# Performance work log

Measured on AMD Instinct MI355X. Metric: run time of the kernel, lower is better.

## Reference

```python
import jax, jax.numpy as jnp
import numpy as np

H = 16   # num_heads
G = 4    # groups (code structurally requires 4)
DIM = 1024
HD = DIM // H // G  # 16


def setup_inputs() -> dict:
    key = jax.random.key(0)
    k1, k2, k3 = jax.random.split(key, 3)
    x = jax.random.normal(k1, (8, 4096, DIM), dtype=jnp.float32)
    w_qkvw = jax.random.normal(k2, (DIM, 4 * DIM), dtype=jnp.float32) * 0.02
    w_out = jax.random.normal(k3, (DIM, DIM), dtype=jnp.float32) * 0.02
    return {"x": x, "w_qkvw": w_qkvw, "w_out": w_out}


def reference(x, w_qkvw, w_out):
    B, S, dim = x.shape
    qkvw = x @ w_qkvw  # [B, S, 4*dim]
    # chunk into G groups along last dim -> G tensors of [B, S, dim] (G==4)
    chunks = jnp.split(qkvw, G, axis=-1)
    # each chunk split again into G sub-chunks of [B, S, dim/G]
    subs = [jnp.split(t, G, axis=-1) for t in chunks]
    # torch: q,k,v,w = [cat([qi,ki,vi,wi], dim=0) for qi,ki,vi,wi in zip(*subs)]
    q = jnp.concatenate([subs[i][0] for i in range(4)], axis=0)  # [4B, S, dim/G]
    k = jnp.concatenate([subs[i][1] for i in range(4)], axis=0)
    v = jnp.concatenate([subs[i][2] for i in range(4)], axis=0)
    w = jnp.concatenate([subs[i][3] for i in range(4)], axis=0)
    # faithful row-major reshape: [4B, S, dim/G] -> [4B, H, S, hd] -> transpose(1,2)
    def shp(t):
        return t.reshape(B * G, H, -1, HD).swapaxes(1, 2)  # [4B, S, H, hd]
    q, k, v = shp(q), shp(k), shp(v)
    w = w.reshape(B * G, H, -1, HD)  # [4B, H, S, hd]
    scale = HD ** -0.5
    scores = (q @ k.swapaxes(-2, -1)) * scale          # [4B, S, H, H]
    attn = jax.nn.softmax(scores, axis=-1)
    o = (attn @ v).swapaxes(1, 2).reshape(B, S, dim)   # [B, S, dim]
    return (o * w.reshape(B, S, dim)) @ w_out
```

## Files before the change

kernel.cpp:

```cpp
#include <hip/hip_runtime.h>
#include <hip/hip_bf16.h>
#include <stdint.h>


typedef __bf16 bf16;
typedef __bf16 bf16x8 __attribute__((ext_vector_type(8)));
typedef float f32x4 __attribute__((ext_vector_type(4)));

__device__ __forceinline__ void gload16(const bf16* g, bf16* l) {
  __builtin_amdgcn_global_load_lds(
      (const __attribute__((address_space(1))) void*)g,
      (__attribute__((address_space(3))) void*)l, 16, 0, 0);
}

#define BAR() asm volatile("s_barrier" ::: "memory")
#define SB() __builtin_amdgcn_sched_barrier(0)
#define LGKM0 asm volatile("s_waitcnt lgkmcnt(0)" ::: "memory")
#define VM4 asm volatile("s_waitcnt vmcnt(4)" ::: "memory")
#define VM0 asm volatile("s_waitcnt vmcnt(0)" ::: "memory")
#define PRIO1 __builtin_amdgcn_s_setprio(1)
#define PRIO0 __builtin_amdgcn_s_setprio(0)

#define READ_A8(dst, base, mq)                                                \
  {                                                                           \
    _Pragma("unroll") for (int i = 0; i < 4; ++i)                             \
        _Pragma("unroll") for (int kk = 0; kk < 2; ++kk)                      \
            dst[i][kk] = *(const bf16x8*)(lds + (base) + ahalf +              \
                                          ((mq)*64 + i * 16 + fr) * 128 +     \
                                          ((kk * 64 + fkb) ^ xo));            \
  }
#define READ_B4(base, nh)                                                     \
  {                                                                           \
    _Pragma("unroll") for (int j2 = 0; j2 < 2; ++j2)                          \
        _Pragma("unroll") for (int kk = 0; kk < 2; ++kk)                      \
            b[(nh)*2 + j2][kk] = *(const bf16x8*)(lds + (base) + bhalf +      \
                                                  (bro + (nh)*32 + j2 * 16 + fr) * 128 + \
                                                  ((kk * 64 + fkb) ^ xo));    \
  }
#define MFMA_Q(arr, mq, nh)                                                   \
  {                                                                           \
    _Pragma("unroll") for (int i = 0; i < 4; ++i)                             \
        _Pragma("unroll") for (int j2 = 0; j2 < 2; ++j2) {                    \
      acc[(mq)*4 + i][(nh)*2 + j2] = __builtin_amdgcn_mfma_f32_16x16x32_bf16( \
          arr[i][0], b[(nh)*2 + j2][0], acc[(mq)*4 + i][(nh)*2 + j2], 0, 0, 0); \
      acc[(mq)*4 + i][(nh)*2 + j2] = __builtin_amdgcn_mfma_f32_16x16x32_bf16( \
          arr[i][1], b[(nh)*2 + j2][1], acc[(mq)*4 + i][(nh)*2 + j2], 0, 0, 0); \
    }                                                                         \
  }
#define STAGE(gsrc, lbase)                                                    \
  {                                                                           \
    gload16((gsrc), (bf16*)(lds + (lbase) + wv * 1024));                      \
    gload16((gsrc) + 64 * 1024, (bf16*)(lds + (lbase) + 8192 + wv * 1024));   \
  }

template <typename OutT>
__global__ __launch_bounds__(512, 2)
void gemm256(const bf16* __restrict__ A, const bf16* __restrict__ BT,
             OutT* __restrict__ C, int N, int super) {
  constexpr int K = 1024;
  __shared__ __align__(16) char smem[131072];
  char* lds = smem;

  const int tid = threadIdx.x;
  const int lane = tid & 63;
  const int wv = tid >> 6;
  const int wr = wv >> 2;
  const int wc = wv & 3;

  const int gx = gridDim.x;
  const int nwg = gx * gridDim.y;
  const int bid = blockIdx.y * gx + blockIdx.x;
  const int xcd = bid & 7;
  const int l = bid >> 3;
  long trow, tcol;
  if (super) {
    const int s = l >> 5, i = l & 31;
    const int colS = gx >> 2;
    trow = xcd * 16 + (s / colS) * 8 + (i >> 2);
    tcol = (s % colS) * 4 + (i & 3);
  } else {
    const int swz = xcd * (nwg >> 3) + l;
    trow = swz / gx;
    tcol = swz % gx;
  }
  const long row0 = trow * 256;
  const long col0 = tcol * 256;

  const int srow = tid >> 3;
  const int scol = (((tid & 7) * 16) ^ ((srow & 7) << 4)) >> 1;
  const bf16* gA = A + (row0 + srow) * K + scol;
  const bf16* gB = BT + (col0 + srow) * K + scol;

  const int fr = lane & 15;
  const int fkb = (lane >> 4) * 16;
  const int xo = (fr & 7) << 4;
  const int bro = (wc & 1) * 64;
  const int ahalf = wr * 16384;
  const int bhalf = (wc >> 1) * 16384;

  bf16x8 a0[4][2], a1[4][2], b[4][2];
  f32x4 acc[8][4] = {};

  STAGE(gA, 0); STAGE(gA + 131072, 16384);
  STAGE(gB, 65536); STAGE(gB + 131072, 81920);
  STAGE(gA + 64, 32768); STAGE(gA + 131072 + 64, 49152);
  VM4;
  SB(); BAR(); SB();

  const bf16* gAm = gA;
  const bf16* gBm = gB;
  for (int j = 0; j < 8; ++j) {
    const bool nl = (j < 7);
    READ_A8(a0, 0, 0); READ_B4(65536, 0);
    STAGE(gBm + 64, 98304);
    SB(); BAR(); LGKM0; SB();
    PRIO1; MFMA_Q(a0, 0, 0); PRIO0; SB(); BAR();
    READ_A8(a1, 0, 1);
    STAGE(gBm + 131072 + 64, 114688);
    SB(); BAR(); LGKM0; SB();
    PRIO1; MFMA_Q(a1, 1, 0); PRIO0; SB(); BAR();
    READ_B4(65536, 1);
    if (nl) STAGE(gAm + 128, 0);
    SB(); BAR(); LGKM0; SB();
    PRIO1; MFMA_Q(a1, 1, 1); PRIO0; SB(); BAR();
    if (nl) {
      STAGE(gAm + 131072 + 128, 16384);
      VM4;
    } else {
      VM0;
    }
    SB(); BAR(); LGKM0; SB();
    PRIO1; MFMA_Q(a0, 0, 1); PRIO0; SB(); BAR();
    READ_A8(a0, 32768, 0); READ_B4(98304, 0);
    if (nl) STAGE(gBm + 128, 65536);
    SB(); BAR(); LGKM0; SB();
    PRIO1; MFMA_Q(a0, 0, 0); PRIO0; SB(); BAR();
    READ_A8(a1, 32768, 1);
    if (nl) STAGE(gBm + 131072 + 128, 81920);
    SB(); BAR(); LGKM0; SB();
    PRIO1; MFMA_Q(a1, 1, 0); PRIO0; SB(); BAR();
    READ_B4(98304, 1);
    if (nl) STAGE(gAm + 192, 32768);
    SB(); BAR(); LGKM0; SB();
    PRIO1; MFMA_Q(a1, 1, 1); PRIO0; SB(); BAR();
    if (nl) {
      STAGE(gAm + 131072 + 192, 49152);
      VM4;
    }
    SB(); BAR(); LGKM0; SB();
    PRIO1; MFMA_Q(a0, 0, 1); PRIO0; SB(); BAR();
    gAm += 128;
    gBm += 128;
  }

  const int crow = (lane >> 4) * 4;
  const int ccol = lane & 15;
  const long rb = row0 + wr * 128;
  const long cb = col0 + wc * 64;
#pragma unroll
  for (int m = 0; m < 8; ++m)
#pragma unroll
    for (int n = 0; n < 4; ++n)
#pragma unroll
      for (int i = 0; i < 4; ++i)
        C[(rb + m * 16 + crow + i) * (long)N + cb + n * 16 + ccol] =
            (OutT)acc[m][n][i];
}

__device__ __forceinline__ void load16f(const bf16* p, float* f) {
  const uint4* u = (const uint4*)p;
  uint4 a = u[0], b = u[1];
  uint32_t w[8] = {a.x, a.y, a.z, a.w, b.x, b.y, b.z, b.w};
#pragma unroll
  for (int j = 0; j < 8; ++j) {
    f[2 * j] = __uint_as_float(w[j] << 16);
    f[2 * j + 1] = __uint_as_float(w[j] & 0xffff0000u);
  }
}

__global__ __launch_bounds__(256)
void attn_fuse(const bf16* __restrict__ qkvw, bf16* __restrict__ ow,
               int b0, long bstride) {
  __shared__ bf16 data[16 * 1024];
  const int s_hi = blockIdx.x;
  const int g = blockIdx.y;
  const int bz = blockIdx.z;
  const int b = b0 + bz;
  const bf16* base = qkvw + (long)bz * bstride;
  const int tid = threadIdx.x;

#pragma unroll
  for (int i = 0; i < 8; ++i) {
    int c = tid + i * 256;
    int h = c >> 7;
    int col = (c & 127) * 8;
    *(uint4*)&data[h * 1024 + col] =
        *(const uint4*)(base + (long)(h * 256 + s_hi) * 4096 + g * 1024 + col);
  }
  __syncthreads();

  const int s_lo = tid >> 4;
  const int h1 = tid & 15;
  const int off = s_lo * 16;

  float q[16], p[16], o[16];
  load16f(&data[h1 * 1024 + off], q);

  float mx = -1e30f;
#pragma unroll
  for (int h2 = 0; h2 < 16; ++h2) {
    float kf[16];
    load16f(&data[h2 * 1024 + 256 + off], kf);
    float s = 0.f;
#pragma unroll
    for (int d = 0; d < 16; ++d) s += q[d] * kf[d];
    s *= 0.25f;
    p[h2] = s;
    mx = fmaxf(mx, s);
  }
  float sum = 0.f;
#pragma unroll
  for (int h2 = 0; h2 < 16; ++h2) {
    float e = __expf(p[h2] - mx);
    p[h2] = e;
    sum += e;
  }
  const float inv = 1.f / sum;
#pragma unroll
  for (int d = 0; d < 16; ++d) o[d] = 0.f;
#pragma unroll
  for (int h2 = 0; h2 < 16; ++h2) {
    float vf[16];
    load16f(&data[h2 * 1024 + 512 + off], vf);
    const float av = p[h2] * inv;
#pragma unroll
    for (int d = 0; d < 16; ++d) o[d] += av * vf[d];
  }
  float wf[16];
  load16f(&data[h1 * 1024 + 768 + off], wf);

  const int bp = g * 8 + b;
  const long R = (long)(bp >> 2) * 4096 + (bp & 3) * 1024 + h1 * 64 + (s_hi >> 2);
  const int cbo = (s_hi & 3) * 256 + off;
  union { uint4 u[2]; bf16 hh[16]; } st;
#pragma unroll
  for (int d = 0; d < 16; ++d) st.hh[d] = (bf16)(o[d] * wf[d]);
  uint4* dst = (uint4*)&ow[R * 1024 + cbo];
  dst[0] = st.u[0];
  dst[1] = st.u[1];
}

__global__ __launch_bounds__(256)
void cast_x_kernel(const float* __restrict__ in, bf16* __restrict__ out, long n4) {
  long i = (long)blockIdx.x * 256 + threadIdx.x;
  if (i >= n4) return;
  float4 v = ((const float4*)in)[i];
  union { uint2 d; bf16 h[4]; } r;
  r.h[0] = (bf16)v.x; r.h[1] = (bf16)v.y; r.h[2] = (bf16)v.z; r.h[3] = (bf16)v.w;
  ((uint2*)out)[i] = r.d;
}

__global__ __launch_bounds__(256)
void tcast_kernel(const float* __restrict__ in, bf16* __restrict__ out, int R, int C) {
  __shared__ float t[64][65];
  const int c0 = blockIdx.x * 64, r0 = blockIdx.y * 64;
  const int lr = threadIdx.x >> 6;
  const int lc = threadIdx.x & 63;
#pragma unroll
  for (int i = 0; i < 16; ++i)
    t[lr + i * 4][lc] = in[(long)(r0 + lr + i * 4) * C + c0 + lc];
  __syncthreads();
#pragma unroll
  for (int i = 0; i < 16; ++i) {
    int oc = lr + i * 4;
    out[(long)(c0 + oc) * R + r0 + lc] = (bf16)t[lc][oc];
  }
}

extern "C" void kernel_launch(void* const* d_in, const int* in_sizes, int n_in,
                              void* d_out, int out_size, void* d_ws, size_t ws_size,
                              hipStream_t stream) {
  const float* x = (const float*)d_in[0];
  const float* w_qkvw = (const float*)d_in[1];
  const float* w_out = (const float*)d_in[2];
  float* out = (float*)d_out;

  char* ws = (char*)d_ws;
  size_t off = 0;
  bf16* x_bf = (bf16*)(ws + off); off += (size_t)32768 * 1024 * 2;
  bf16* bt1  = (bf16*)(ws + off); off += (size_t)4096 * 1024 * 2;
  bf16* bt2  = (bf16*)(ws + off); off += (size_t)1024 * 1024 * 2;
  bf16* owb  = (bf16*)(ws + off); off += (size_t)32768 * 1024 * 2;
  bf16* qk   = (bf16*)(ws + off);
  const size_t rem = ws_size > off ? ws_size - off : 0;
  const size_t full_need = (size_t)32768 * 4096 * 2;

  cast_x_kernel<<<32768, 256, 0, stream>>>(x, x_bf, (long)8388608);
  tcast_kernel<<<dim3(64, 16), 256, 0, stream>>>(w_qkvw, bt1, 1024, 4096);
  tcast_kernel<<<dim3(16, 16), 256, 0, stream>>>(w_out, bt2, 1024, 1024);

  if (rem >= full_need) {
    gemm256<bf16><<<dim3(16, 128), 512, 0, stream>>>(x_bf, bt1, qk, 4096, 1);
    attn_fuse<<<dim3(256, 4, 8), 256, 0, stream>>>(qk, owb, 0, (long)4096 * 4096);
  } else {
    for (int b = 0; b < 8; ++b) {
      gemm256<bf16><<<dim3(16, 16), 512, 0, stream>>>(
          x_bf + (size_t)b * 4096 * 1024, bt1, qk, 4096, 0);
      attn_fuse<<<dim3(256, 4, 1), 256, 0, stream>>>(qk, owb, b, 0);
    }
  }
  gemm256<float><<<dim3(4, 128), 512, 0, stream>>>(owb, bt2, out, 1024, 1);
}
```

Baseline: 462.7 us.

## Switch GEMM inner loop from 16x16x32 to 32x32x16 MFMA tiles

```diff
diff --git a/kernel.cpp b/kernel.cpp
--- a/kernel.cpp
+++ b/kernel.cpp
@@ -5,7 +5,7 @@
 
 typedef __bf16 bf16;
 typedef __bf16 bf16x8 __attribute__((ext_vector_type(8)));
-typedef float f32x4 __attribute__((ext_vector_type(4)));
+typedef float f32x16 __attribute__((ext_vector_type(16)));
 
 __device__ __forceinline__ void gload16(const bf16* g, bf16* l) {
   __builtin_amdgcn_global_load_lds(
@@ -23,29 +23,25 @@
 
 #define READ_A8(dst, base, mq)                                                \
   {                                                                           \
-    _Pragma("unroll") for (int i = 0; i < 4; ++i)                             \
-        _Pragma("unroll") for (int kk = 0; kk < 2; ++kk)                      \
-            dst[i][kk] = *(const bf16x8*)(lds + (base) + ahalf +              \
-                                          ((mq)*64 + i * 16 + fr) * 128 +     \
-                                          ((kk * 64 + fkb) ^ xo));            \
-  }
-#define READ_B4(base, nh)                                                     \
+    _Pragma("unroll") for (int i = 0; i < 2; ++i)                             \
+        _Pragma("unroll") for (int ks = 0; ks < 4; ++ks)                      \
+            dst[i][ks] = *(const bf16x8*)(lds + (base) + ahalf +              \
+                                          ((mq)*64 + i * 32 + arow) * 128 +   \
+                                          ((ks * 32 + fkb) ^ xo));            \
+  }
+#define READ_B4(dst, base, nh)                                                \
   {                                                                           \
-    _Pragma("unroll") for (int j2 = 0; j2 < 2; ++j2)                          \
-        _Pragma("unroll") for (int kk = 0; kk < 2; ++kk)                      \
-            b[(nh)*2 + j2][kk] = *(const bf16x8*)(lds + (base) + bhalf +      \
-                                                  (bro + (nh)*32 + j2 * 16 + fr) * 128 + \
-                                                  ((kk * 64 + fkb) ^ xo));    \
-  }
-#define MFMA_Q(arr, mq, nh)                                                   \
+    _Pragma("unroll") for (int ks = 0; ks < 4; ++ks)                          \
+        dst[ks] = *(const bf16x8*)(lds + (base) + bhalf +                     \
+                                   (bro + (nh)*32 + arow) * 128 +             \
+                                   ((ks * 32 + fkb) ^ xo));                   \
+  }
+#define MFMA_Q(arr, bv, mq)                                                   \
   {                                                                           \
-    _Pragma("unroll") for (int i = 0; i < 4; ++i)                             \
-        _Pragma("unroll") for (int j2 = 0; j2 < 2; ++j2) {                    \
-      acc[(mq)*4 + i][(nh)*2 + j2] = __builtin_amdgcn_mfma_f32_16x16x32_bf16( \
-          arr[i][0], b[(nh)*2 + j2][0], acc[(mq)*4 + i][(nh)*2 + j2], 0, 0, 0); \
-      acc[(mq)*4 + i][(nh)*2 + j2] = __builtin_amdgcn_mfma_f32_16x16x32_bf16( \
-          arr[i][1], b[(nh)*2 + j2][1], acc[(mq)*4 + i][(nh)*2 + j2], 0, 0, 0); \
-    }                                                                         \
+    _Pragma("unroll") for (int ks = 0; ks < 4; ++ks)                          \
+        _Pragma("unroll") for (int i = 0; i < 2; ++i)                         \
+            accq[(mq)*2 + i] = __builtin_amdgcn_mfma_f32_32x32x16_bf16(       \
+                arr[i][ks], bv[ks], accq[(mq)*2 + i], 0, 0, 0);               \
   }
 #define STAGE(gsrc, lbase)                                                    \
   {                                                                           \
@@ -91,15 +87,16 @@
   const bf16* gA = A + (row0 + srow) * K + scol;
   const bf16* gB = BT + (col0 + srow) * K + scol;
 
-  const int fr = lane & 15;
-  const int fkb = (lane >> 4) * 16;
-  const int xo = (fr & 7) << 4;
+  const int arow = lane & 31;
+  const int fkb = (lane >> 5) * 16;
+  const int xo = (arow & 7) << 4;
   const int bro = (wc & 1) * 64;
   const int ahalf = wr * 16384;
   const int bhalf = (wc >> 1) * 16384;
 
-  bf16x8 a0[4][2], a1[4][2], b[4][2];
-  f32x4 acc[8][4] = {};
+  bf16x8 a0[2][4], a1[2][4], b0[4], b1[4];
+  f32x16 accq[4] = {};
+  f32x16 accq1[4] = {};
 
   STAGE(gA, 0); STAGE(gA + 131072, 16384);
   STAGE(gB, 65536); STAGE(gB + 131072, 81920);
@@ -111,18 +108,27 @@
   const bf16* gBm = gB;
   for (int j = 0; j < 8; ++j) {
     const bool nl = (j < 7);
-    READ_A8(a0, 0, 0); READ_B4(65536, 0);
+    READ_A8(a0, 0, 0); READ_B4(b0, 65536, 0);
     STAGE(gBm + 64, 98304);
     SB(); BAR(); LGKM0; SB();
-    PRIO1; MFMA_Q(a0, 0, 0); PRIO0; SB(); BAR();
+    PRIO1; MFMA_Q(a0, b0, 0); PRIO0; SB(); BAR();
     READ_A8(a1, 0, 1);
     STAGE(gBm + 131072 + 64, 114688);
     SB(); BAR(); LGKM0; SB();
-    PRIO1; MFMA_Q(a1, 1, 0); PRIO0; SB(); BAR();
-    READ_B4(65536, 1);
+    PRIO1; MFMA_Q(a1, b0, 1); PRIO0; SB(); BAR();
+    READ_B4(b1, 65536, 1);
     if (nl) STAGE(gAm + 128, 0);
     SB(); BAR(); LGKM0; SB();
-    PRIO1; MFMA_Q(a1, 1, 1); PRIO0; SB(); BAR();
+    {
+      f32x16* accq_ = accq1;
+      PRIO1;
+      _Pragma("unroll") for (int ks = 0; ks < 4; ++ks)
+          _Pragma("unroll") for (int i = 0; i < 2; ++i)
+              accq_[2 + i] = __builtin_amdgcn_mfma_f32_32x32x16_bf16(
+                  a1[i][ks], b1[ks], accq_[2 + i], 0, 0, 0);
+      PRIO0;
+    }
+    SB(); BAR();
     if (nl) {
       STAGE(gAm + 131072 + 128, 16384);
       VM4;
@@ -130,41 +136,69 @@
       VM0;
     }
     SB(); BAR(); LGKM0; SB();
-    PRIO1; MFMA_Q(a0, 0, 1); PRIO0; SB(); BAR();
-    READ_A8(a0, 32768, 0); READ_B4(98304, 0);
+    {
+      f32x16* accq_ = accq1;
+      PRIO1;
+      _Pragma("unroll") for (int ks = 0; ks < 4; ++ks)
+          _Pragma("unroll") for (int i = 0; i < 2; ++i)
+              accq_[i] = __builtin_amdgcn_mfma_f32_32x32x16_bf16(
+                  a0[i][ks], b1[ks], accq_[i], 0, 0, 0);
+      PRIO0;
+    }
+    SB(); BAR();
+    READ_A8(a0, 32768, 0); READ_B4(b0, 98304, 0);
     if (nl) STAGE(gBm + 128, 65536);
     SB(); BAR(); LGKM0; SB();
-    PRIO1; MFMA_Q(a0, 0, 0); PRIO0; SB(); BAR();
+    PRIO1; MFMA_Q(a0, b0, 0); PRIO0; SB(); BAR();
     READ_A8(a1, 32768, 1);
     if (nl) STAGE(gBm + 131072 + 128, 81920);
     SB(); BAR(); LGKM0; SB();
-    PRIO1; MFMA_Q(a1, 1, 0); PRIO0; SB(); BAR();
-    READ_B4(98304, 1);
+    PRIO1; MFMA_Q(a1, b0, 1); PRIO0; SB(); BAR();
+    READ_B4(b1, 98304, 1);
     if (nl) STAGE(gAm + 192, 32768);
     SB(); BAR(); LGKM0; SB();
-    PRIO1; MFMA_Q(a1, 1, 1); PRIO0; SB(); BAR();
+    {
+      f32x16* accq_ = accq1;
+      PRIO1;
+      _Pragma("unroll") for (int ks = 0; ks < 4; ++ks)
+          _Pragma("unroll") for (int i = 0; i < 2; ++i)
+              accq_[2 + i] = __builtin_amdgcn_mfma_f32_32x32x16_bf16(
+                  a1[i][ks], b1[ks], accq_[2 + i], 0, 0, 0);
+      PRIO0;
+    }
+    SB(); BAR();
     if (nl) {
       STAGE(gAm + 131072 + 192, 49152);
       VM4;
     }
     SB(); BAR(); LGKM0; SB();
-    PRIO1; MFMA_Q(a0, 0, 1); PRIO0; SB(); BAR();
+    {
+      f32x16* accq_ = accq1;
+      PRIO1;
+      _Pragma("unroll") for (int ks = 0; ks < 4; ++ks)
+          _Pragma("unroll") for (int i = 0; i < 2; ++i)
+              accq_[i] = __builtin_amdgcn_mfma_f32_32x32x16_bf16(
+                  a0[i][ks], b1[ks], accq_[i], 0, 0, 0);
+      PRIO0;
+    }
+    SB(); BAR();
     gAm += 128;
     gBm += 128;
   }
 
-  const int crow = (lane >> 4) * 4;
-  const int ccol = lane & 15;
+  const int ccol = lane & 31;
+  const int rbase = 4 * (lane >> 5);
   const long rb = row0 + wr * 128;
   const long cb = col0 + wc * 64;
 #pragma unroll
-  for (int m = 0; m < 8; ++m)
-#pragma unroll
-    for (int n = 0; n < 4; ++n)
-#pragma unroll
-      for (int i = 0; i < 4; ++i)
-        C[(rb + m * 16 + crow + i) * (long)N + cb + n * 16 + ccol] =
-            (OutT)acc[m][n][i];
+  for (int mt = 0; mt < 4; ++mt) {
+#pragma unroll
+    for (int reg = 0; reg < 16; ++reg) {
+      const long r = rb + mt * 32 + rbase + (reg & 3) + 8 * (reg >> 2);
+      C[r * (long)N + cb + ccol] = (OutT)accq[mt][reg];
+      C[r * (long)N + cb + 32 + ccol] = (OutT)accq1[mt][reg];
+    }
+  }
 }
 
 __device__ __forceinline__ void load16f(const bf16* p, float* f) {
```

Measured after the change: 497.2 us. +7.5%, slower.

## Restructure GEMM main loop pipeline with double-buffered B fragments and rotated MFMA order

Applied to the files above, without the earlier changes.

```diff
diff --git a/kernel.cpp b/kernel.cpp
--- a/kernel.cpp
+++ b/kernel.cpp
@@ -13,10 +13,10 @@
       (__attribute__((address_space(3))) void*)l, 16, 0, 0);
 }
 
-#define BAR() asm volatile("s_barrier" ::: "memory")
+#define BAR() __builtin_amdgcn_s_barrier()
 #define SB() __builtin_amdgcn_sched_barrier(0)
 #define LGKM0 asm volatile("s_waitcnt lgkmcnt(0)" ::: "memory")
-#define VM4 asm volatile("s_waitcnt vmcnt(4)" ::: "memory")
+#define VM6 asm volatile("s_waitcnt vmcnt(6)" ::: "memory")
 #define VM0 asm volatile("s_waitcnt vmcnt(0)" ::: "memory")
 #define PRIO1 __builtin_amdgcn_s_setprio(1)
 #define PRIO0 __builtin_amdgcn_s_setprio(0)
@@ -29,22 +29,22 @@
                                           ((mq)*64 + i * 16 + fr) * 128 +     \
                                           ((kk * 64 + fkb) ^ xo));            \
   }
-#define READ_B4(base, nh)                                                     \
+#define READ_B4(dst, base, nh)                                                \
   {                                                                           \
     _Pragma("unroll") for (int j2 = 0; j2 < 2; ++j2)                          \
         _Pragma("unroll") for (int kk = 0; kk < 2; ++kk)                      \
-            b[(nh)*2 + j2][kk] = *(const bf16x8*)(lds + (base) + bhalf +      \
-                                                  (bro + (nh)*32 + j2 * 16 + fr) * 128 + \
-                                                  ((kk * 64 + fkb) ^ xo));    \
-  }
-#define MFMA_Q(arr, mq, nh)                                                   \
+            dst[j2][kk] = *(const bf16x8*)(lds + (base) + bhalf +             \
+                                           (bro + (nh)*32 + j2 * 16 + fr) * 128 + \
+                                           ((kk * 64 + fkb) ^ xo));           \
+  }
+#define MFMA_Q(arr, bv, mq, nh)                                               \
   {                                                                           \
     _Pragma("unroll") for (int i = 0; i < 4; ++i)                             \
         _Pragma("unroll") for (int j2 = 0; j2 < 2; ++j2) {                    \
       acc[(mq)*4 + i][(nh)*2 + j2] = __builtin_amdgcn_mfma_f32_16x16x32_bf16( \
-          arr[i][0], b[(nh)*2 + j2][0], acc[(mq)*4 + i][(nh)*2 + j2], 0, 0, 0); \
+          arr[i][0], bv[j2][0], acc[(mq)*4 + i][(nh)*2 + j2], 0, 0, 0);       \
       acc[(mq)*4 + i][(nh)*2 + j2] = __builtin_amdgcn_mfma_f32_16x16x32_bf16( \
-          arr[i][1], b[(nh)*2 + j2][1], acc[(mq)*4 + i][(nh)*2 + j2], 0, 0, 0); \
+          arr[i][1], bv[j2][1], acc[(mq)*4 + i][(nh)*2 + j2], 0, 0, 0);       \
     }                                                                         \
   }
 #define STAGE(gsrc, lbase)                                                    \
@@ -98,60 +98,71 @@
   const int ahalf = wr * 16384;
   const int bhalf = (wc >> 1) * 16384;
 
-  bf16x8 a0[4][2], a1[4][2], b[4][2];
+  bf16x8 a0[4][2], a1[4][2], bn0[2][2], bn1[2][2];
   f32x4 acc[8][4] = {};
 
   STAGE(gA, 0); STAGE(gA + 131072, 16384);
   STAGE(gB, 65536); STAGE(gB + 131072, 81920);
-  STAGE(gA + 64, 32768); STAGE(gA + 131072 + 64, 49152);
-  VM4;
-  SB(); BAR(); SB();
+  STAGE(gB + 64, 98304); STAGE(gB + 131072 + 64, 114688);
+  STAGE(gA + 64, 32768);
+  VM6;
+  BAR();
 
   const bf16* gAm = gA;
   const bf16* gBm = gB;
   for (int j = 0; j < 8; ++j) {
     const bool nl = (j < 7);
-    READ_A8(a0, 0, 0); READ_B4(65536, 0);
-    STAGE(gBm + 64, 98304);
-    SB(); BAR(); LGKM0; SB();
-    PRIO1; MFMA_Q(a0, 0, 0); PRIO0; SB(); BAR();
+    READ_B4(bn0, 65536, 0);
+    STAGE(gAm + 131072 + 64, 49152);
+    BAR(); LGKM0; SB();
+    if (j) { PRIO1; MFMA_Q(a1, bn1, 1, 1); PRIO0; }
+    BAR();
+    READ_A8(a0, 0, 0);
+    READ_B4(bn1, 65536, 1);
+    BAR(); LGKM0; SB();
+    PRIO1; MFMA_Q(a0, bn0, 0, 0); PRIO0;
+    BAR();
     READ_A8(a1, 0, 1);
-    STAGE(gBm + 131072 + 64, 114688);
-    SB(); BAR(); LGKM0; SB();
-    PRIO1; MFMA_Q(a1, 1, 0); PRIO0; SB(); BAR();
-    READ_B4(65536, 1);
-    if (nl) STAGE(gAm + 128, 0);
-    SB(); BAR(); LGKM0; SB();
-    PRIO1; MFMA_Q(a1, 1, 1); PRIO0; SB(); BAR();
+    if (nl) { STAGE(gBm + 128, 65536); STAGE(gBm + 131072 + 128, 81920); }
+    BAR(); LGKM0; SB();
+    PRIO1; MFMA_Q(a1, bn0, 1, 0); PRIO0;
+    BAR();
     if (nl) {
-      STAGE(gAm + 131072 + 128, 16384);
-      VM4;
+      STAGE(gAm + 128, 0);
+      VM6;
     } else {
       VM0;
     }
-    SB(); BAR(); LGKM0; SB();
-    PRIO1; MFMA_Q(a0, 0, 1); PRIO0; SB(); BAR();
-    READ_A8(a0, 32768, 0); READ_B4(98304, 0);
-    if (nl) STAGE(gBm + 128, 65536);
-    SB(); BAR(); LGKM0; SB();
-    PRIO1; MFMA_Q(a0, 0, 0); PRIO0; SB(); BAR();
+    BAR(); LGKM0; SB();
+    PRIO1; MFMA_Q(a0, bn1, 0, 1); PRIO0;
+    BAR();
+    READ_B4(bn0, 98304, 0);
+    if (nl) STAGE(gAm + 131072 + 128, 16384);
+    BAR(); LGKM0; SB();
+    PRIO1; MFMA_Q(a1, bn1, 1, 1); PRIO0;
+    BAR();
+    READ_A8(a0, 32768, 0);
+    READ_B4(bn1, 98304, 1);
+    BAR(); LGKM0; SB();
+    PRIO1; MFMA_Q(a0, bn0, 0, 0); PRIO0;
+    BAR();
     READ_A8(a1, 32768, 1);
-    if (nl) STAGE(gBm + 131072 + 128, 81920);
-    SB(); BAR(); LGKM0; SB();
-    PRIO1; MFMA_Q(a1, 1, 0); PRIO0; SB(); BAR();
-    READ_B4(98304, 1);
-    if (nl) STAGE(gAm + 192, 32768);
-    SB(); BAR(); LGKM0; SB();
-    PRIO1; MFMA_Q(a1, 1, 1); PRIO0; SB(); BAR();
+    if (nl) STAGE(gBm + 192, 98304);
+    BAR(); LGKM0; SB();
+    PRIO1; MFMA_Q(a1, bn0, 1, 0); PRIO0;
+    BAR();
     if (nl) {
-      STAGE(gAm + 131072 + 192, 49152);
-      VM4;
+      STAGE(gBm + 131072 + 192, 114688);
+      STAGE(gAm + 192, 32768);
+      VM6;
     }
-    SB(); BAR(); LGKM0; SB();
-    PRIO1; MFMA_Q(a0, 0, 1); PRIO0; SB(); BAR();
+    BAR(); LGKM0; SB();
+    PRIO1; MFMA_Q(a0, bn1, 0, 1); PRIO0;
+    BAR();
     gAm += 128;
     gBm += 128;
   }
+  PRIO1; MFMA_Q(a1, bn1, 1, 1); PRIO0;
 
   const int crow = (lane >> 4) * 4;
   const int ccol = lane & 15;
```

New measurement: 506.2 us. 1.09x slower.
